# Optimization experiments

Hardware: AMD Instinct MI355X
Metric: run time of the kernel (lower is better)

Reference implementation:

```python
import jax, jax.numpy as jnp
import numpy as np
from jax import lax

D_MODEL = 256; D_HEAD = 32; NHEAD = 8; WIN = 8; TOPK = 8; DMID = 1024
B = 2; H = 128; WD = 128
BN_EPS = 1e-5; ATT_EPS = 1e-6

def _bn(x, g, b, m, v):
    # inference-mode BatchNorm2d over NCHW
    s = g / jnp.sqrt(v + BN_EPS)
    return x * s[None, :, None, None] + (b - m * s)[None, :, None, None]

def _gelu(x):
    return jax.nn.gelu(x, approximate=False)  # torch nn.GELU default (erf)

def _conv1x1(x, w, bias=None):
    y = jnp.einsum('bchw,oc->bohw', x, w)
    if bias is not None:
        y = y + bias[None, :, None, None]
    return y

def _to_win(t):
    b, d, h, wd = t.shape
    nh, nw = h // WIN, wd // WIN
    t = t.reshape(b, d, nh, WIN, nw, WIN).transpose(0, 2, 4, 3, 5, 1)
    return t.reshape(b, nh * nw, WIN * WIN, d)

def _from_win(m, h, wd):
    b, n, w2, d = m.shape
    nh, nw = h // WIN, wd // WIN
    m = m.reshape(b, nh, nw, WIN, WIN, d).transpose(0, 5, 1, 3, 2, 4)
    return m.reshape(b, d, h, wd)

def _linear_attention(q, k, v):
    # LoFTR linear attention. q: [n, L, H, D]; k, v: [n, S, H, D]
    Q = jax.nn.elu(q) + 1.0
    K = jax.nn.elu(k) + 1.0
    s_len = v.shape[1]
    vals = v / s_len
    KV = jnp.einsum('nshd,nshv->nhdv', K, vals)
    Z = 1.0 / (jnp.einsum('nlhd,nhd->nlh', Q, K.sum(axis=1)) + ATT_EPS)
    return jnp.einsum('nlhd,nhdv,nlh->nlhv', Q, KV, Z) * s_len

def _topk_window_attention(q, k, v):
    # partition into WINxWIN windows, select top-K key windows per query window
    # by mean-pooled window similarity, gather them, attend within each window.
    b, d, h, wd = q.shape
    qw, kw, vw = _to_win(q), _to_win(k), _to_win(v)  # [b, N, W2, d]
    n = qw.shape[1]; w2 = WIN * WIN
    sim = jnp.einsum('bnd,bmd->bnm', qw.mean(axis=2), kw.mean(axis=2))
    idx = lax.top_k(sim, TOPK)[1]  # [b, N, K]
    gather = jax.vmap(lambda t, i: t[i])  # over batch: [N,W2,d],[N,K] -> [N,K,W2,d]
    kg = gather(kw, idx).reshape(b, n, TOPK * w2, d)
    vg = gather(vw, idx).reshape(b, n, TOPK * w2, d)
    Q = qw.reshape(b * n, w2, NHEAD, D_HEAD)
    K = kg.reshape(b * n, TOPK * w2, NHEAD, D_HEAD)
    V = vg.reshape(b * n, TOPK * w2, NHEAD, D_HEAD)
    out = _linear_attention(Q, K, V).reshape(b, n, w2, d)
    return _from_win(out, h, wd)

def _forward(x0, bn0_g, bn0_b, bn0_m, bn0_v, q_w, k_w, v_w, merge_w, merge_b,
             mlp_w1, bn1_g, bn1_b, bn1_m, bn1_v, mlp_dw,
             bn2_g, bn2_b, bn2_m, bn2_v, mlp_w2, bn3_g, bn3_b, bn3_m, bn3_v):
    _x = _gelu(_bn(x0, bn0_g, bn0_b, bn0_m, bn0_v))  # pre_normact (x1 = x0)
    q = _conv1x1(_x, q_w); k = _conv1x1(_x, k_w); v = _conv1x1(_x, v_w)
    msg = _topk_window_attention(q, k, v)
    x = x0 + _conv1x1(msg, merge_w, merge_b)  # merge + residual (DropPath=id)
    # MB mlp block: 1x1 -> BN -> GELU -> dw3x3 -> BN -> GELU -> 1x1 -> BN
    y = _conv1x1(x, mlp_w1)
    y = _gelu(_bn(y, bn1_g, bn1_b, bn1_m, bn1_v))
    y = lax.conv_general_dilated(y, mlp_dw, (1, 1), 'SAME',
                                 feature_group_count=DMID,
                                 dimension_numbers=('NCHW', 'OIHW', 'NCHW'))
    y = _gelu(_bn(y, bn2_g, bn2_b, bn2_m, bn2_v))
    y = _conv1x1(y, mlp_w2)
    y = _bn(y, bn3_g, bn3_b, bn3_m, bn3_v)
    return x + y

def setup_inputs() -> dict:
    ks = jax.random.split(jax.random.key(0), 26)
    nrm = lambda i, shape, s=1.0: jax.random.normal(ks[i], shape, jnp.float32) * s
    uni = lambda i, shape: jax.random.uniform(ks[i], shape, jnp.float32, 0.5, 1.5)
    sc = float(1.0 / np.sqrt(D_MODEL))
    return {
        'x0': nrm(0, (B, D_MODEL, H, WD)),
        'bn0_g': uni(1, (D_MODEL,)), 'bn0_b': nrm(2, (D_MODEL,), 0.1),
        'bn0_m': nrm(3, (D_MODEL,), 0.1), 'bn0_v': uni(4, (D_MODEL,)),
        'q_w': nrm(5, (D_MODEL, D_MODEL), sc),
        'k_w': nrm(6, (D_MODEL, D_MODEL), sc),
        'v_w': nrm(7, (D_MODEL, D_MODEL), sc),
        'merge_w': nrm(8, (D_MODEL, D_MODEL), sc), 'merge_b': nrm(9, (D_MODEL,), 0.1),
        'mlp_w1': nrm(10, (DMID, D_MODEL), sc),
        'bn1_g': uni(11, (DMID,)), 'bn1_b': nrm(12, (DMID,), 0.1),
        'bn1_m': nrm(13, (DMID,), 0.1), 'bn1_v': uni(14, (DMID,)),
        'mlp_dw': nrm(15, (DMID, 1, 3, 3), 1.0 / 3.0),
        'bn2_g': uni(16, (DMID,)), 'bn2_b': nrm(17, (DMID,), 0.1),
        'bn2_m': nrm(18, (DMID,), 0.1), 'bn2_v': uni(19, (DMID,)),
        'mlp_w2': nrm(20, (D_MODEL, DMID), float(1.0 / np.sqrt(DMID))),
        'bn3_g': uni(21, (D_MODEL,)), 'bn3_b': nrm(22, (D_MODEL,), 0.1),
        'bn3_m': nrm(23, (D_MODEL,), 0.1), 'bn3_v': uni(24, (D_MODEL,)),
    }

def reference(x0, bn0_g, bn0_b, bn0_m, bn0_v, q_w, k_w, v_w, merge_w, merge_b,
              mlp_w1, bn1_g, bn1_b, bn1_m, bn1_v, mlp_dw,
              bn2_g, bn2_b, bn2_m, bn2_v, mlp_w2, bn3_g, bn3_b, bn3_m, bn3_v):
    return _forward(x0, bn0_g, bn0_b, bn0_m, bn0_v, q_w, k_w, v_w, merge_w, merge_b,
                    mlp_w1, bn1_g, bn1_b, bn1_m, bn1_v, mlp_dw,
                    bn2_g, bn2_b, bn2_m, bn2_v, mlp_w2, bn3_g, bn3_b, bn3_m, bn3_v)
```

## Files before the change

kernel.cpp:

```cpp
#include <hip/hip_runtime.h>
#include <hip/hip_bf16.h>
#include <type_traits>

typedef __hip_bfloat16 bf16;
typedef __attribute__((ext_vector_type(8))) short s16x8;
typedef __attribute__((ext_vector_type(4))) short s16x4;
typedef __attribute__((ext_vector_type(4))) float f32x4;

#define DEVI __device__ __forceinline__

DEVI float bf2f(bf16 x) { return __bfloat162float(x); }
DEVI float to_f(float x) { return x; }
DEVI float to_f(bf16 x) { return __bfloat162float(x); }
DEVI float gelu_f(float x) {
  const float y = x * 0.7071067811865476f;
  const float a = fabsf(y);
  const float t = __builtin_amdgcn_rcpf(1.0f + 0.3275911f * a);
  const float p = t * (0.254829592f + t * (-0.284496736f +
                  t * (1.421413741f + t * (-1.453152027f + t * 1.061405429f))));
  const float e = __expf(-a * a);
  const float erfv = copysignf(1.0f - p * e, y);
  return 0.5f * x * (1.0f + erfv);
}
DEVI float elu1(float x) { return x > 0.f ? x + 1.f : __expf(x); }
DEVI float s2f(short s) {
  unsigned u = ((unsigned)(unsigned short)s) << 16;
  float f; __builtin_memcpy(&f, &u, 4); return f;
}
DEVI short f2s(float x) {
  bf16 h = __float2bfloat16(x);
  short s; __builtin_memcpy(&s, &h, 2); return s;
}

__global__ void detect_kernel(const void* x0, int* dflag) {
  const int t = threadIdx.x;
  const bf16* p = (const bf16*)x0;
  float v = bf2f(p[t * 2]);
  bool ok = (fabsf(v) <= 64.0f);
  unsigned long long m = __ballot(ok);
  if (t == 0) dflag[0] = (m == ~0ull) ? 0 : 1;
}

template <typename TIN>
__global__ __launch_bounds__(256) void bnprep_kernel(
    const int* dflag, int want,
    const TIN* g0, const TIN* b0, const TIN* m0, const TIN* v0,
    const TIN* g1, const TIN* b1, const TIN* m1, const TIN* v1,
    const TIN* g2, const TIN* b2, const TIN* m2, const TIN* v2,
    const TIN* g3, const TIN* b3, const TIN* m3, const TIN* v3,
    const TIN* mb, float* out)
{
  if (want >= 0 && dflag[0] != want) return;
  int t = threadIdx.x;
  {
    float s = to_f(g0[t]) / sqrtf(to_f(v0[t]) + 1e-5f);
    out[t] = s; out[256 + t] = to_f(b0[t]) - to_f(m0[t]) * s;
  }
  for (int i = t; i < 1024; i += 256) {
    float s = to_f(g1[i]) / sqrtf(to_f(v1[i]) + 1e-5f);
    out[512 + i] = s; out[1536 + i] = to_f(b1[i]) - to_f(m1[i]) * s;
  }
  for (int i = t; i < 1024; i += 256) {
    float s = to_f(g2[i]) / sqrtf(to_f(v2[i]) + 1e-5f);
    out[2560 + i] = s; out[3584 + i] = to_f(b2[i]) - to_f(m2[i]) * s;
  }
  {
    float s = to_f(g3[t]) / sqrtf(to_f(v3[t]) + 1e-5f);
    out[4608 + t] = s; out[4864 + t] = to_f(b3[t]) - to_f(m3[t]) * s;
    out[5120 + t] = to_f(mb[t]);
  }
}

template <typename TIN>
__global__ __launch_bounds__(256) void wconv_kernel(
    const int* dflag, int want,
    const TIN* qw, const TIN* kw, const TIN* vw, const TIN* mw,
    const TIN* w1, const TIN* w2, const TIN* dw, bf16* dst)
{
  if (want >= 0 && dflag[0] != want) return;
  int i = blockIdx.x * 256 + threadIdx.x;
  if (i >= 795648) return;
  const TIN* src; int off;
  if (i < 262144) {
    src = (i < 65536) ? qw : (i < 131072) ? kw : (i < 196608) ? vw : mw;
    off = i & 65535;
  } else if (i < 524288) { src = w1; off = i - 262144; }
  else if (i < 786432) { src = w2; off = i - 524288; }
  else {
    src = dw;
    const int o = i - 786432;
    const int tap = o >> 10, m = o & 1023;
    off = m * 9 + tap;
    if (o >= 9216) return;
  }
  dst[i] = __float2bfloat16(to_f(src[off]));
}

template <typename TIN>
__global__ __launch_bounds__(256) void prenorm_t_kernel(
    const int* dflag, int want, const TIN* __restrict__ x0,
    const float* __restrict__ bn, bf16* __restrict__ xhat_t,
    float* __restrict__ xmp)
{
  if (want >= 0 && dflag[0] != want) return;
  __shared__ float T[128][67];
  const int t = threadIdx.x;
  const int tile = blockIdx.x;
  const int b = tile >> 8;
  const int rc = tile & 255;
  const int p0 = rc * 64;
  const int row = rc >> 1, colh = rc & 1;
  const int win = (row >> 3) * 16 + colh * 8 + (t & 7);
  const int wrow = row & 7;
  const long xbase = (long)b * 4194304 + p0;
  const int px_off = (t & 7) * 8;
  const int chr = t >> 3;
  const int ch8 = (t & 15) * 8;
  const int pxw = t >> 4;
  #pragma unroll
  for (int pass = 0; pass < 2; ++pass) {
    const int Hc = pass * 128;
    __syncthreads();
    #pragma unroll
    for (int cc = 0; cc < 4; ++cc) {
      const int ch = Hc + chr + 32 * cc;
      const TIN* xp = x0 + (long)ch * 16384 + xbase + px_off;
      float v[8];
      if constexpr (sizeof(TIN) == 2) {
        const s16x8 r = *(const s16x8*)xp;
        #pragma unroll
        for (int j = 0; j < 8; ++j) v[j] = s2f(r[j]);
      } else {
        const float4 a = *(const float4*)xp;
        const float4 c = *(const float4*)(xp + 4);
        v[0] = a.x; v[1] = a.y; v[2] = a.z; v[3] = a.w;
        v[4] = c.x; v[5] = c.y; v[6] = c.z; v[7] = c.w;
      }
      const float s0 = bn[ch], t0 = bn[256 + ch];
      #pragma unroll
      for (int j = 0; j < 8; ++j) v[j] = gelu_f(v[j] * s0 + t0);
      float s8 = v[0];
      #pragma unroll
      for (int j = 1; j < 8; ++j) s8 += v[j];
      xmp[(((b * 8 + wrow) * 256 + ch) << 8) + win] = s8;
      float* Tr = &T[chr + 32 * cc][px_off];
      #pragma unroll
      for (int j = 0; j < 8; ++j) Tr[j] = v[j];
    }
    __syncthreads();
    #pragma unroll
    for (int it = 0; it < 4; ++it) {
      const int px = pxw + 16 * it;
      alignas(16) short o[8];
      #pragma unroll
      for (int j = 0; j < 8; ++j) o[j] = f2s(T[ch8 + j][px]);
      *(uint4*)(xhat_t + (long)(b * 16384 + p0 + px) * 256 + Hc + ch8) =
          *(const uint4*)o;
    }
  }
}

__global__ __launch_bounds__(256) void xred_kernel(const float* __restrict__ xmp,
                                                   float* __restrict__ xm)
{
  const int tid = blockIdx.x * 256 + threadIdx.x;
  const int nw = tid & 255, c = (tid >> 8) & 255, b = tid >> 16;
  float s = 0.f;
  #pragma unroll
  for (int w = 0; w < 8; ++w)
    s += xmp[(((b * 8 + w) * 256 + c) << 8) + nw];
  xm[tid] = s * 0.015625f;
}

template <int MODE, typename TRES = bf16>
__global__ __launch_bounds__(256) void mfma_gemm(
    const int* dflag, int want, int isfp,
    const bf16* __restrict__ in, const bf16* __restrict__ w,
    void* __restrict__ out, long obase, const void* __restrict__ resv,
    const float* __restrict__ sv, const float* __restrict__ tv,
    float* __restrict__ aux, int N, int M, int K)
{
  if (want >= 0 && dflag[0] != want) return;
  alignas(16) __shared__ char smem[(MODE == 0 || MODE == 2) ? 20480 : 34816];
  bf16* inT = (bf16*)smem;
  bf16* wT  = (bf16*)(smem + 10240);
  const int t = threadIdx.x;
  const int n0 = blockIdx.x * 128, m0 = blockIdx.y * 128;
  const int sr = t >> 1, sk = (t & 1) * 16;
  const int wid = t >> 6, lane = t & 63;
  const int nw = (wid & 1) * 64, mw = (wid >> 1) * 64;
  const int l15 = lane & 15, quad = lane >> 4;
  f32x4 acc[4][4];
  #pragma unroll
  for (int i = 0; i < 4; ++i)
    #pragma unroll
    for (int j = 0; j < 4; ++j) acc[i][j] = 0.f;
  long inRow;
  if (MODE == 4) {
    const int bb4 = n0 >> 14, w0 = (n0 & 16383) >> 6;
    const int win = w0 + (sr >> 6);
    const int rr = (sr >> 3) & 7, cc = sr & 7;
    inRow = ((long)(bb4 * 16384 + ((win >> 4) * 8 + rr) * 128
                    + (win & 15) * 8 + cc)) * K + sk;
  } else {
    inRow = (long)(n0 + sr) * K + sk;
  }
  const long wRow = (long)(m0 + sr) * K + sk;
  uint4 a0 = *(const uint4*)(in + inRow);
  uint4 a1 = *(const uint4*)(in + inRow + 8);
  uint4 b0 = *(const uint4*)(w + wRow);
  uint4 b1 = *(const uint4*)(w + wRow + 8);
  for (int k0 = 0; k0 < K; k0 += 32) {
    __syncthreads();
    *(uint4*)(inT + sr * 40 + sk) = a0;
    *(uint4*)(inT + sr * 40 + sk + 8) = a1;
    *(uint4*)(wT + sr * 40 + sk) = b0;
    *(uint4*)(wT + sr * 40 + sk + 8) = b1;
    __syncthreads();
    if (k0 + 32 < K) {
      a0 = *(const uint4*)(in + inRow + k0 + 32);
      a1 = *(const uint4*)(in + inRow + k0 + 40);
      b0 = *(const uint4*)(w + wRow + k0 + 32);
      b1 = *(const uint4*)(w + wRow + k0 + 40);
    }
    s16x8 af[4], bfv[4];
    #pragma unroll
    for (int i = 0; i < 4; ++i)
      af[i] = *(const s16x8*)(inT + (nw + i * 16 + l15) * 40 + quad * 8);
    #pragma unroll
    for (int i = 0; i < 4; ++i)
      bfv[i] = *(const s16x8*)(wT + (mw + i * 16 + l15) * 40 + quad * 8);
    #pragma unroll
    for (int i = 0; i < 4; ++i)
      #pragma unroll
      for (int j = 0; j < 4; ++j)
        acc[i][j] = __builtin_amdgcn_mfma_f32_16x16x32_bf16(af[i], bfv[j], acc[i][j], 0, 0, 0);
  }
  if (MODE == 0 || MODE == 2) {
    bf16* ob = (bf16*)out;
    const bool doelu = (MODE == 0) && (m0 < 512);
    #pragma unroll
    for (int i = 0; i < 4; ++i) {
      #pragma unroll
      for (int r = 0; r < 4; ++r) {
        const int n = n0 + nw + i * 16 + quad * 4 + r;
        #pragma unroll
        for (int j = 0; j < 4; ++j) {
          const int m = m0 + mw + j * 16 + l15;
          float vv = acc[i][j][r];
          if (MODE == 0) { if (doelu) vv = elu1(vv); }
          if (MODE == 2) vv = gelu_f(vv * sv[m] + tv[m]);
          ob[(long)n * M + m] = __float2bfloat16(vv);
        }
      }
    }
  } else if (MODE == 1) {
    __syncthreads();
    bf16* xL = (bf16*)smem;
    {
      const int bb = n0 >> 14, nloc = n0 & 16383;
      const int chl = t >> 1, pxh = (t & 1) * 64;
      const TRES* xp = (const TRES*)resv + (long)bb * 4194304
                     + (long)(m0 + chl) * 16384 + nloc + pxh;
      alignas(16) short tmp[64];
      if constexpr (std::is_same<TRES, float>::value) {
        #pragma unroll
        for (int q = 0; q < 16; ++q) {
          const float4 f = *(const float4*)(xp + q * 4);
          tmp[q * 4 + 0] = f2s(f.x); tmp[q * 4 + 1] = f2s(f.y);
          tmp[q * 4 + 2] = f2s(f.z); tmp[q * 4 + 3] = f2s(f.w);
        }
      } else {
        #pragma unroll
        for (int q = 0; q < 8; ++q)
          *(s16x8*)(tmp + q * 8) = *(const s16x8*)((const bf16*)xp + q * 8);
      }
      bf16* xd = xL + chl * 132 + pxh;
      #pragma unroll
      for (int q = 0; q < 8; ++q)
        *(uint4*)(xd + q * 8) = *(const uint4*)(tmp + q * 8);
    }
    __syncthreads();
    bf16* ob = (bf16*)out;
    #pragma unroll
    for (int i = 0; i < 4; ++i)
      #pragma unroll
      for (int r = 0; r < 4; ++r) {
        const int nl = nw + i * 16 + quad * 4 + r;
        const int n = n0 + nl;
        #pragma unroll
        for (int j = 0; j < 4; ++j) {
          const int ml = mw + j * 16 + l15;
          const int m = m0 + ml;
          const float vv = acc[i][j][r] + sv[m] + bf2f(xL[ml * 132 + nl]);
          ob[(long)n * 256 + m] = __float2bfloat16(vv);
        }
      }
  } else {
    const int isf = (MODE == 3) ? (isfp >= 0 ? isfp : dflag[0]) : 0;
    __syncthreads();
    bf16* T = (bf16*)smem;
    #pragma unroll
    for (int i = 0; i < 4; ++i)
      #pragma unroll
      for (int r = 0; r < 4; ++r) {
        const int n = nw + i * 16 + quad * 4 + r;
        #pragma unroll
        for (int j = 0; j < 4; ++j) {
          const int m = mw + j * 16 + l15;
          float vv = acc[i][j][r];
          if (MODE == 3)
            vv = vv * sv[m0 + m] + tv[m0 + m]
               + bf2f(((const bf16*)resv)[(long)(n0 + n) * 256 + m0 + m]);
          else { if (m0 + m < 256) vv = elu1(vv); }
          T[m * 136 + n] = __float2bfloat16(vv);
        }
      }
    __syncthreads();
    const int mr = t >> 1, half = (t & 1) * 64;
    if (MODE == 4) {
      const int bb4 = n0 >> 14, w0 = (n0 & 16383) >> 6;
      const int gm = m0 + mr;
      bf16* bo = (bf16*)out;
      #pragma unroll
      for (int jj = 0; jj < 8; ++jj) {
        const int C = half + jj * 8;
        const int win = w0 + (C >> 6);
        const int pxc = (C & 63) >> 3;
        *(uint4*)(bo + ((long)(bb4 * 256 + win) << 15) + pxc * 4096 + gm * 8) =
            *(const uint4*)(T + mr * 136 + C);
      }
      if (m0 < 256) {
        float s = 0.f;
        const bf16* Tr = T + mr * 136 + half;
        #pragma unroll
        for (int c8 = 0; c8 < 8; ++c8) {
          const s16x8 v = *(const s16x8*)(Tr + c8 * 8);
          #pragma unroll
          for (int e = 0; e < 8; ++e) s += s2f(v[e]);
        }
        aux[(long)(bb4 * 256 + w0 + (half >> 6)) * 256 + gm] = s;
      }
    } else {
      const int bb3 = n0 >> 14, nloc = n0 & 16383;
      if (!isf) {
        bf16* bo = (bf16*)out + obase + (long)bb3 * 4194304;
        #pragma unroll
        for (int jj = 0; jj < 8; ++jj)
          *(uint4*)(bo + (long)(m0 + mr) * 16384 + nloc + half + jj * 8) =
              *(const uint4*)(T + mr * 136 + half + jj * 8);
      } else {
        float* fo = (float*)out + obase + (long)bb3 * 4194304;
        #pragma unroll
        for (int jj = 0; jj < 8; ++jj)
          #pragma unroll
          for (int e = 0; e < 8; ++e)
            fo[(long)(m0 + mr) * 16384 + nloc + half + jj * 8 + e] =
                bf2f(T[mr * 136 + half + jj * 8 + e]);
      }
    }
  }
}

template <typename TIN>
__global__ __launch_bounds__(256) void meanproj_kernel(const int* dflag, int want,
    const TIN* __restrict__ qw, const TIN* __restrict__ kw,
    const float* __restrict__ xm, float* __restrict__ qm, float* __restrict__ km)
{
  if (want >= 0 && dflag[0] != want) return;
  int tid = blockIdx.x * 256 + threadIdx.x;
  int nw = tid & 255, o = (tid >> 8) & 255, b = tid >> 16;
  float q0 = 0.f, q1 = 0.f, q2 = 0.f, q3 = 0.f;
  float k0 = 0.f, k1 = 0.f, k2 = 0.f, k3 = 0.f;
  for (int c = 0; c < 256; c += 4) {
    const float x0v = xm[((b * 256 + c) << 8) + nw];
    const float x1v = xm[((b * 256 + c + 1) << 8) + nw];
    const float x2v = xm[((b * 256 + c + 2) << 8) + nw];
    const float x3v = xm[((b * 256 + c + 3) << 8) + nw];
    q0 += to_f(qw[o * 256 + c]) * x0v;     k0 += to_f(kw[o * 256 + c]) * x0v;
    q1 += to_f(qw[o * 256 + c + 1]) * x1v; k1 += to_f(kw[o * 256 + c + 1]) * x1v;
    q2 += to_f(qw[o * 256 + c + 2]) * x2v; k2 += to_f(kw[o * 256 + c + 2]) * x2v;
    q3 += to_f(qw[o * 256 + c + 3]) * x3v; k3 += to_f(kw[o * 256 + c + 3]) * x3v;
  }
  qm[((b * 256 + o) << 8) + nw] = (q0 + q1) + (q2 + q3);
  km[((b * 256 + o) << 8) + nw] = (k0 + k1) + (k2 + k3);
}

__global__ __launch_bounds__(256) void topk_kernel(const float* __restrict__ qm,
                                                   const float* __restrict__ km,
                                                   int* __restrict__ topki)
{
  const int nq = blockIdx.x, b = blockIdx.y, t = threadIdx.x;
  const int lane = t & 63, wid = t >> 6;
  float sim = 0.f;
  for (int c = 0; c < 256; ++c)
    sim += qm[((b * 256 + c) << 8) + nq] * km[((b * 256 + c) << 8) + t];
  __shared__ float vals[256];
  __shared__ float rv4[4];
  __shared__ int ri4[4];
  vals[t] = sim;
  __syncthreads();
  for (int j = 0; j < 8; ++j) {
    float v = vals[t]; int idx = t;
    #pragma unroll
    for (int off = 1; off < 64; off <<= 1) {
      const float v2 = __shfl_xor(v, off);
      const int i2 = __shfl_xor(idx, off);
      if (v2 > v || (v2 == v && i2 < idx)) { v = v2; idx = i2; }
    }
    if (lane == 0) { rv4[wid] = v; ri4[wid] = idx; }
    __syncthreads();
    float bv = rv4[0]; int bi = ri4[0];
    #pragma unroll
    for (int w2 = 1; w2 < 4; ++w2)
      if (rv4[w2] > bv || (rv4[w2] == bv && ri4[w2] < bi)) { bv = rv4[w2]; bi = ri4[w2]; }
    if (t == 0) topki[(b * 256 + nq) * 8 + j] = bi;
    if (t == bi) vals[t] = -3.0e38f;
    __syncthreads();
  }
}

__global__ __launch_bounds__(256) void attn_kernel(
    const bf16* __restrict__ qbuf, const bf16* __restrict__ kvT,
    const int* __restrict__ topki, const float* __restrict__ S,
    bf16* __restrict__ msg)
{
  __shared__ bf16 kvB[10240];
  __shared__ float ksum_s[256];
  __shared__ float zs2[512];
  const int n = blockIdx.x, b = blockIdx.y, t = threadIdx.x;
  const long bpix = (long)b * 16384;
  const int lane = t & 63, wid = t >> 6;
  const int l15 = lane & 15, quad = lane >> 4;
  const int h0 = wid * 2;
  f32x4 kvacc[2][2][2];
  #pragma unroll
  for (int a = 0; a < 2; ++a)
    #pragma unroll
    for (int c = 0; c < 2; ++c)
      #pragma unroll
      for (int d = 0; d < 2; ++d) kvacc[a][c][d] = 0.f;
  int wsel[8];
  #pragma unroll
  for (int j = 0; j < 8; ++j) wsel[j] = topki[(b * 256 + n) * 8 + j];

  const long kvTb = (long)b * 8388608;
  #pragma unroll 8
  for (int ck = 0; ck < 16; ++ck) {
    const bf16* base = kvT + kvTb + ((long)wsel[ck >> 1] << 15)
                     + ((ck & 1) * 4 + quad) * 4096;
    #pragma unroll
    for (int hs = 0; hs < 2; ++hs) {
      const int cb = (h0 + hs) * 32;
      const s16x8 a0 = *(const s16x8*)(base + (cb + l15) * 8);
      const s16x8 a1 = *(const s16x8*)(base + (cb + 16 + l15) * 8);
      const s16x8 b0 = *(const s16x8*)(base + (256 + cb + l15) * 8);
      const s16x8 b1 = *(const s16x8*)(base + (256 + cb + 16 + l15) * 8);
      kvacc[hs][0][0] = __builtin_amdgcn_mfma_f32_16x16x32_bf16(a0, b0, kvacc[hs][0][0], 0, 0, 0);
      kvacc[hs][0][1] = __builtin_amdgcn_mfma_f32_16x16x32_bf16(a0, b1, kvacc[hs][0][1], 0, 0, 0);
      kvacc[hs][1][0] = __builtin_amdgcn_mfma_f32_16x16x32_bf16(a1, b0, kvacc[hs][1][0], 0, 0, 0);
      kvacc[hs][1][1] = __builtin_amdgcn_mfma_f32_16x16x32_bf16(a1, b1, kvacc[hs][1][1], 0, 0, 0);
    }
  }

  {
    float ks = 0.f;
    #pragma unroll
    for (int j = 0; j < 8; ++j)
      ks += S[((long)b * 256 + wsel[j]) * 256 + t];
    ksum_s[t] = ks;
  }
  #pragma unroll
  for (int hs = 0; hs < 2; ++hs)
    #pragma unroll
    for (int vt = 0; vt < 2; ++vt) {
      const int row = (h0 + hs) * 32 + vt * 16 + l15;
      #pragma unroll
      for (int dt = 0; dt < 2; ++dt) {
        const f32x4 kv = kvacc[hs][dt][vt];
        uint2 u;
        u.x = (unsigned)(unsigned short)f2s(kv[0])
            | ((unsigned)(unsigned short)f2s(kv[1]) << 16);
        u.y = (unsigned)(unsigned short)f2s(kv[2])
            | ((unsigned)(unsigned short)f2s(kv[3]) << 16);
        *(uint2*)(kvB + row * 40 + dt * 16 + quad * 4) = u;
      }
    }
  __syncthreads();

  const int qh0 = (n >> 4) * 8, qw0 = (n & 15) * 8;
  #pragma unroll
  for (int rep = 0; rep < 2; ++rep) {
    const int idx = t + rep * 256;
    const int l = idx >> 3, hh = idx & 7;
    const long gp = bpix + (qh0 + (l >> 3)) * 128 + qw0 + (l & 7);
    const bf16* qp = qbuf + gp * 256 + hh * 32;
    float dot = 0.f;
    #pragma unroll
    for (int k4 = 0; k4 < 4; ++k4) {
      const s16x8 q8 = *(const s16x8*)(qp + k4 * 8);
      const float4 kA = *(const float4*)(ksum_s + hh * 32 + k4 * 8);
      const float4 kB = *(const float4*)(ksum_s + hh * 32 + k4 * 8 + 4);
      dot += s2f(q8[0]) * kA.x + s2f(q8[1]) * kA.y
           + s2f(q8[2]) * kA.z + s2f(q8[3]) * kA.w
           + s2f(q8[4]) * kB.x + s2f(q8[5]) * kB.y
           + s2f(q8[6]) * kB.z + s2f(q8[7]) * kB.w;
    }
    zs2[hh * 64 + l] = 1.f / (dot + 1e-6f);
  }
  __syncthreads();

  #pragma unroll
  for (int hs = 0; hs < 2; ++hs) {
    const int h = h0 + hs;
    const s16x8 B0 = *(const s16x8*)(kvB + (h * 32 + l15) * 40 + quad * 8);
    const s16x8 B1 = *(const s16x8*)(kvB + (h * 32 + 16 + l15) * 40 + quad * 8);
    #pragma unroll
    for (int i = 0; i < 4; ++i) {
      const int lq = i * 16 + l15;
      const long gpa = bpix + (qh0 + (lq >> 3)) * 128 + qw0 + (lq & 7);
      const s16x8 A = *(const s16x8*)(qbuf + gpa * 256 + h * 32 + quad * 8);
      f32x4 o0 = 0.f, o1 = 0.f;
      o0 = __builtin_amdgcn_mfma_f32_16x16x32_bf16(A, B0, o0, 0, 0, 0);
      o1 = __builtin_amdgcn_mfma_f32_16x16x32_bf16(A, B1, o1, 0, 0, 0);
      const float4 z4 = *(const float4*)(zs2 + h * 64 + i * 16 + quad * 4);
      const float zr[4] = {z4.x, z4.y, z4.z, z4.w};
      #pragma unroll
      for (int r = 0; r < 4; ++r) {
        const int lo = i * 16 + quad * 4 + r;
        const long opix = bpix + (qh0 + (lo >> 3)) * 128 + qw0 + (lo & 7);
        msg[opix * 256 + h * 32 + l15] = __float2bfloat16(o0[r] * zr[r]);
        msg[opix * 256 + h * 32 + 16 + l15] = __float2bfloat16(o1[r] * zr[r]);
      }
    }
  }
}

__global__ __launch_bounds__(256) void dwconv_kernel(const bf16* __restrict__ y1,
                                                     const bf16* __restrict__ wdw,
                                                     const float* __restrict__ s2,
                                                     const float* __restrict__ t2,
                                                     bf16* __restrict__ y2)
{
  const int strip = blockIdx.x;
  const int bb = strip >> 11;
  const int sl = strip & 2047;
  const int x0 = (sl & 15) * 8;
  const int yy = sl >> 4;
  const int m0 = threadIdx.x * 4;
  const bf16* y1b = y1 + (long)bb * 16777216;
  bf16* y2b = y2 + (long)bb * 16777216;
  float wv[9][4];
  #pragma unroll
  for (int tap = 0; tap < 9; ++tap) {
    const s16x4 w4 = *(const s16x4*)(wdw + tap * 1024 + m0);
    #pragma unroll
    for (int e = 0; e < 4; ++e) wv[tap][e] = s2f(w4[e]);
  }
  float acc[8][4];
  #pragma unroll
  for (int p = 0; p < 8; ++p)
    #pragma unroll
    for (int e = 0; e < 4; ++e) acc[p][e] = 0.f;
  #pragma unroll
  for (int ky = 0; ky < 3; ++ky) {
    const int row = yy + ky - 1;
    if ((unsigned)row < 128u) {
      const bf16* rp = y1b + (long)row * 131072 + m0;
      #pragma unroll
      for (int cr = 0; cr < 10; ++cr) {
        const int xc = x0 + cr - 1;
        if ((unsigned)xc < 128u) {
          const s16x4 v4 = *(const s16x4*)(rp + (long)xc * 1024);
          float vf[4];
          #pragma unroll
          for (int e = 0; e < 4; ++e) vf[e] = s2f(v4[e]);
          #pragma unroll
          for (int kx = 0; kx < 3; ++kx) {
            const int p = cr - kx;
            if (p >= 0 && p < 8) {
              #pragma unroll
              for (int e = 0; e < 4; ++e)
                acc[p][e] += wv[ky * 3 + kx][e] * vf[e];
            }
          }
        }
      }
    }
  }
  const float4 sv = *(const float4*)(s2 + m0);
  const float4 tv = *(const float4*)(t2 + m0);
  #pragma unroll
  for (int p = 0; p < 8; ++p) {
    s16x4 o;
    o[0] = f2s(gelu_f(acc[p][0] * sv.x + tv.x));
    o[1] = f2s(gelu_f(acc[p][1] * sv.y + tv.y));
    o[2] = f2s(gelu_f(acc[p][2] * sv.z + tv.z));
    o[3] = f2s(gelu_f(acc[p][3] * sv.w + tv.w));
    *(s16x4*)(y2b + (long)(yy * 128 + x0 + p) * 1024 + m0) = o;
  }
}

template <typename TIN>
static void stage_dtype_pre(int want, void* const* d_in, hipStream_t stream,
                            const int* dflag, bf16* wb, float* bnbuf,
                            bf16* xhat_t, float* xmp)
{
  bnprep_kernel<TIN><<<1, 256, 0, stream>>>(dflag, want,
      (const TIN*)d_in[1],  (const TIN*)d_in[2],  (const TIN*)d_in[3],  (const TIN*)d_in[4],
      (const TIN*)d_in[11], (const TIN*)d_in[12], (const TIN*)d_in[13], (const TIN*)d_in[14],
      (const TIN*)d_in[16], (const TIN*)d_in[17], (const TIN*)d_in[18], (const TIN*)d_in[19],
      (const TIN*)d_in[21], (const TIN*)d_in[22], (const TIN*)d_in[23], (const TIN*)d_in[24],
      (const TIN*)d_in[9], bnbuf);
  wconv_kernel<TIN><<<3108, 256, 0, stream>>>(dflag, want,
      (const TIN*)d_in[5], (const TIN*)d_in[6], (const TIN*)d_in[7], (const TIN*)d_in[8],
      (const TIN*)d_in[10], (const TIN*)d_in[20], (const TIN*)d_in[15], wb);
  prenorm_t_kernel<TIN><<<512, 256, 0, stream>>>(dflag, want,
      (const TIN*)d_in[0], bnbuf, xhat_t, xmp);
}

extern "C" void kernel_launch(void* const* d_in, const int* in_sizes, int n_in,
                              void* d_out, int out_size, void* d_ws, size_t ws_size,
                              hipStream_t stream) {
  (void)n_in; (void)out_size;
  char* W = (char*)d_ws;
  bf16*  xhat_t = (bf16*)(W);
  bf16*  xres   = (bf16*)(W);
  float* Swin   = (float*)(W + 16777216);
  float* xmp    = (float*)(W + 17301504);
  bf16*  qbuf   = (bf16*)(W + 33554432);
  bf16*  kvT    = (bf16*)(W + 50331648);
  bf16*  msg    = (bf16*)(W + 83886080);
  char*  S      = W + 100663296;
  bf16*  wb     = (bf16*)(S);
  bf16*  wmb    = wb + 196608;
  bf16*  w1b    = wb + 262144;
  bf16*  w2b    = wb + 524288;
  bf16*  wdwb   = wb + 786432;
  float* bnbuf  = (float*)(S + 1591296);
  float* xm     = (float*)(S + 1612800);
  float* qm     = (float*)(S + 2137088);
  float* km     = (float*)(S + 2661376);
  int*   topki  = (int*)(S + 3185664);
  int*   dflag  = (int*)(S + 3202048);
  const bool big = (ws_size == 0) || (ws_size >= 171966464ull);
  bf16*  y1     = (bf16*)(W + 33554432);
  bf16*  y2     = big ? (bf16*)(W + 104857600) : (bf16*)(W + 67108864);

  int known = -1;
  if (in_sizes) {
    if (in_sizes[0] == 16777216) known = 0;
    else if (in_sizes[0] == 33554432) known = 1;
  }

  if (known < 0) detect_kernel<<<1, 64, 0, stream>>>(d_in[0], dflag);

  if (known != 1)
    stage_dtype_pre<bf16>(known == 0 ? -1 : 0, d_in, stream, dflag, wb, bnbuf, xhat_t, xmp);
  if (known != 0)
    stage_dtype_pre<float>(known == 1 ? -1 : 1, d_in, stream, dflag, wb, bnbuf, xhat_t, xmp);

  xred_kernel<<<512, 256, 0, stream>>>(xmp, xm);
  if (known != 1)
    meanproj_kernel<bf16><<<512, 256, 0, stream>>>(dflag, known == 0 ? -1 : 0,
        (const bf16*)d_in[5], (const bf16*)d_in[6], xm, qm, km);
  if (known != 0)
    meanproj_kernel<float><<<512, 256, 0, stream>>>(dflag, known == 1 ? -1 : 1,
        (const float*)d_in[5], (const float*)d_in[6], xm, qm, km);

  mfma_gemm<0><<<dim3(256, 2), 256, 0, stream>>>(dflag, -1, -1,
      xhat_t, wb, (void*)qbuf, 0, nullptr, nullptr, nullptr, nullptr, 32768, 256, 256);
  mfma_gemm<4><<<dim3(256, 4), 256, 0, stream>>>(dflag, -1, -1,
      xhat_t, wb + 65536, (void*)kvT, 0, nullptr, nullptr, nullptr, Swin, 32768, 512, 256);

  topk_kernel<<<dim3(256, 2), 256, 0, stream>>>(qm, km, topki);
  attn_kernel<<<dim3(256, 2), 256, 0, stream>>>(qbuf, kvT, topki, Swin, msg);

  if (known != 1)
    mfma_gemm<1, bf16><<<dim3(256, 2), 256, 0, stream>>>(dflag, known == 0 ? -1 : 0, -1,
        msg, wmb, (void*)xres, 0, d_in[0], bnbuf + 5120, nullptr, nullptr, 32768, 256, 256);
  if (known != 0)
    mfma_gemm<1, float><<<dim3(256, 2), 256, 0, stream>>>(dflag, known == 1 ? -1 : 1, -1,
        msg, wmb, (void*)xres, 0, d_in[0], bnbuf + 5120, nullptr, nullptr, 32768, 256, 256);

  if (big) {
    mfma_gemm<2><<<dim3(256, 8), 256, 0, stream>>>(dflag, -1, -1,
        xres, w1b, (void*)y1, 0, nullptr, bnbuf + 512, bnbuf + 1536, nullptr, 32768, 1024, 256);
    dwconv_kernel<<<4096, 256, 0, stream>>>(y1, wdwb, bnbuf + 2560, bnbuf + 3584, y2);
    mfma_gemm<3><<<dim3(256, 2), 256, 0, stream>>>(dflag, -1, known,
        y2, w2b, d_out, 0, xres, bnbuf + 4608, bnbuf + 4864, nullptr, 32768, 256, 1024);
  } else {
    for (int b = 0; b < 2; ++b) {
      bf16* xres_b = xres + (long)b * 4194304;
      mfma_gemm<2><<<dim3(128, 8), 256, 0, stream>>>(dflag, -1, -1,
          xres_b, w1b, (void*)y1, 0, nullptr, bnbuf + 512, bnbuf + 1536, nullptr, 16384, 1024, 256);
      dwconv_kernel<<<2048, 256, 0, stream>>>(y1, wdwb, bnbuf + 2560, bnbuf + 3584, y2);
      mfma_gemm<3><<<dim3(128, 2), 256, 0, stream>>>(dflag, -1, known,
          y2, w2b, d_out, (long)b * 4194304, xres_b,
          bnbuf + 4608, bnbuf + 4864, nullptr, 16384, 256, 1024);
    }
  }
}
```

Before: 389.2 us.

## Double-buffer LDS tiles in MFMA GEMM and vectorize fp32 epilogue stores

The GEMM main loop now uses two LDS buffers. The next K-slice is written into the alternate buffer after the MFMAs, so each iteration needs one barrier instead of two. The fp32 output path also switches from scalar stores to float4 stores. In exchange, shared memory grows to 40KB for every mode, which may reduce occupancy for the modes that used 20KB before.

```diff
diff --git a/kernel.cpp b/kernel.cpp
--- a/kernel.cpp
+++ b/kernel.cpp
@@ -181,9 +181,7 @@
     float* __restrict__ aux, int N, int M, int K)
 {
   if (want >= 0 && dflag[0] != want) return;
-  alignas(16) __shared__ char smem[(MODE == 0 || MODE == 2) ? 20480 : 34816];
-  bf16* inT = (bf16*)smem;
-  bf16* wT  = (bf16*)(smem + 10240);
+  alignas(16) __shared__ char smem[40960];
   const int t = threadIdx.x;
   const int n0 = blockIdx.x * 128, m0 = blockIdx.y * 128;
   const int sr = t >> 1, sk = (t & 1) * 16;
@@ -210,19 +208,26 @@
   uint4 a1 = *(const uint4*)(in + inRow + 8);
   uint4 b0 = *(const uint4*)(w + wRow);
   uint4 b1 = *(const uint4*)(w + wRow + 8);
-  for (int k0 = 0; k0 < K; k0 += 32) {
-    __syncthreads();
+  {
+    bf16* inT = (bf16*)smem;
+    bf16* wT  = (bf16*)(smem + 10240);
     *(uint4*)(inT + sr * 40 + sk) = a0;
     *(uint4*)(inT + sr * 40 + sk + 8) = a1;
     *(uint4*)(wT + sr * 40 + sk) = b0;
     *(uint4*)(wT + sr * 40 + sk + 8) = b1;
-    __syncthreads();
-    if (k0 + 32 < K) {
+  }
+  int ph = 0;
+  for (int k0 = 0; k0 < K; k0 += 32) {
+    __syncthreads();
+    const bool more = (k0 + 32 < K);
+    if (more) {
       a0 = *(const uint4*)(in + inRow + k0 + 32);
       a1 = *(const uint4*)(in + inRow + k0 + 40);
       b0 = *(const uint4*)(w + wRow + k0 + 32);
       b1 = *(const uint4*)(w + wRow + k0 + 40);
     }
+    const bf16* inT = (const bf16*)(smem + ph * 20480);
+    const bf16* wT  = (const bf16*)(smem + ph * 20480 + 10240);
     s16x8 af[4], bfv[4];
     #pragma unroll
     for (int i = 0; i < 4; ++i)
@@ -235,6 +240,15 @@
       #pragma unroll
       for (int j = 0; j < 4; ++j)
         acc[i][j] = __builtin_amdgcn_mfma_f32_16x16x32_bf16(af[i], bfv[j], acc[i][j], 0, 0, 0);
+    if (more) {
+      bf16* inT2 = (bf16*)(smem + (ph ^ 1) * 20480);
+      bf16* wT2  = (bf16*)(smem + (ph ^ 1) * 20480 + 10240);
+      *(uint4*)(inT2 + sr * 40 + sk) = a0;
+      *(uint4*)(inT2 + sr * 40 + sk + 8) = a1;
+      *(uint4*)(wT2 + sr * 40 + sk) = b0;
+      *(uint4*)(wT2 + sr * 40 + sk + 8) = b1;
+    }
+    ph ^= 1;
   }
   if (MODE == 0 || MODE == 2) {
     bf16* ob = (bf16*)out;
@@ -352,11 +366,17 @@
       } else {
         float* fo = (float*)out + obase + (long)bb3 * 4194304;
         #pragma unroll
-        for (int jj = 0; jj < 8; ++jj)
-          #pragma unroll
-          for (int e = 0; e < 8; ++e)
-            fo[(long)(m0 + mr) * 16384 + nloc + half + jj * 8 + e] =
-                bf2f(T[mr * 136 + half + jj * 8 + e]);
+        for (int jj = 0; jj < 8; ++jj) {
+          const bf16* Tr = T + mr * 136 + half + jj * 8;
+          float4 f0, f1;
+          f0.x = bf2f(Tr[0]); f0.y = bf2f(Tr[1]);
+          f0.z = bf2f(Tr[2]); f0.w = bf2f(Tr[3]);
+          f1.x = bf2f(Tr[4]); f1.y = bf2f(Tr[5]);
+          f1.z = bf2f(Tr[6]); f1.w = bf2f(Tr[7]);
+          float* fd = fo + (long)(m0 + mr) * 16384 + nloc + half + jj * 8;
+          *(float4*)fd = f0;
+          *(float4*)(fd + 4) = f1;
+        }
       }
     }
   }
```

New measurement: 394.3 us. No clear change (+1.3%).
